# Optimization experiments

Measured on AMD Instinct MI355X. Metric: run time of the kernel, lower is better.

## Reference

```python
import jax, jax.numpy as jnp
import numpy as np

NUM_BITS = 2
QN = -(2 ** (NUM_BITS - 1))          # -2 (signed)
QP = 2 ** (NUM_BITS - 1) - 1         # 1
NUM_LEVELS = 2 ** NUM_BITS           # 4


def setup_inputs() -> dict:
    key = jax.random.key(0)
    k1, k2 = jax.random.split(key)
    # Large transformer FFN weight matrix: d_model=4096, d_ff=16384
    weights = jax.random.normal(k1, (4096, 16384), dtype=jnp.float32) * 0.1
    alpha = jax.random.uniform(k2, (1,), dtype=jnp.float32, minval=0.05, maxval=0.2)
    return {"weights": weights, "alpha": alpha}


def reference(weights, alpha):
    # backprop_to_alpha=False -> alpha is detached everywhere (torch uses .item())
    a = jax.lax.stop_gradient(alpha[0])
    w = weights.reshape(-1)

    # LSQ quantization levels: [Qn*a, ..., -a, 0, a, ..., Qp*a]
    levels = jnp.arange(QN, QP + 1, dtype=w.dtype) * a            # [NUM_LEVELS]

    # Bin assignment by LSQ integer code (non-differentiable indices)
    bins = jnp.round(jnp.clip(w / a, QN, QP)).astype(jnp.int32)   # in [QN, QP]
    idx = bins - QN                                               # in [0, NUM_LEVELS)

    # Single-pass per-bin sum / sumsq / count (replaces per-bin mask loop)
    count = jax.ops.segment_sum(jnp.ones_like(w), idx, num_segments=NUM_LEVELS)
    s = jax.ops.segment_sum(w, idx, num_segments=NUM_LEVELS)
    sq = jax.ops.segment_sum(w * w, idx, num_segments=NUM_LEVELS)

    safe = jnp.maximum(count, 1.0)
    mean = s / safe
    var = sq / safe - mean * mean                                 # biased (unbiased=False)

    total_mse = jnp.sum(jnp.where(count > 0, (mean - levels) ** 2, 0.0))
    total_var = jnp.sum(jnp.where(count >= 2, var, 0.0))
    loss = total_mse + total_var

    # Diagnostics (computed under no_grad in torch)
    wq = bins.astype(w.dtype) * a                                 # quantized weights
    d = jax.lax.stop_gradient(w - wq)
    mean_distance = jnp.mean(jnp.abs(d))
    quantization_mse = jnp.mean(d * d)

    return jnp.stack([loss, total_mse, total_var, quantization_mse, mean_distance])
```

## Files before the change

### kernel.cpp

```cpp
#include <hip/hip_runtime.h>
#include <cstdint>

#define TS 16384
#define NSLOT 16
#define NCH 7
#define NPART 1024
#define PBT 256
#define FLQ 1024


__device__ __forceinline__ int kbin_th(float x, double T1, double T2) {
    double xd = (double)x;
    if (xd >   T1) return 1;
    if (xd >= -T1) return 0;
    if (xd >  -T2) return -1;
    return -2;
}

__device__ __forceinline__ double wred64(double v) {
#pragma unroll
    for (int d = 32; d >= 1; d >>= 1) v += __shfl_xor(v, d, 64);
    return v;
}
__device__ __forceinline__ int wred32i(int v) {
#pragma unroll
    for (int d = 32; d >= 1; d >>= 1) v += __shfl_xor(v, d, 64);
    return v;
}

__device__ __forceinline__ int expo_bits(double A) {
    const long long b = __double_as_longlong(A);
    return (int)((b >> 52) & 0x7FF) - 1023;
}
__device__ __forceinline__ int emin_of(double A0) {
    if (!(A0 > 0.0)) return 12345;
    const int e = expo_bits(A0);
    if (e < -100 || e > 100) return 12345;
    return e;
}

__global__ __launch_bounds__(64) void zero2(double* __restrict__ diag,
        float* __restrict__ chains, double* __restrict__ A0d) {
    if (threadIdx.x < 8) {
        diag[threadIdx.x] = 0.0;
        chains[threadIdx.x] = 0.0f;
        A0d[threadIdx.x] = 0.0;
    }
}

__global__ __launch_bounds__(PBT) void part1(const float* __restrict__ w,
        const float* __restrict__ alpha, int* __restrict__ hist,
        double* __restrict__ diag, long long n, long long nseg)
{
    const float a = alpha[0];
    const double T1 = (double)a * (0.5 + 0x1p-25);
    const double T2 = (double)a * (1.5 - 0x1p-24);
    const long long seg = (long long)blockIdx.x * nseg;
    long long send = seg + nseg; if (send > n) send = n;
    int h0=0,h1=0,h2=0,h3=0;
    double ad=0.0, dd=0.0, s0=0.0;

    for (long long i = seg + (long long)threadIdx.x*4; i < send; i += PBT*4) {
        float4 v;
        if (i + 3 < send) v = *reinterpret_cast<const float4*>(w + i);
        else {
            v = make_float4(0.f,0.f,0.f,0.f);
            v.x = w[i];
            if (i+1 < send) v.y = w[i+1];
            if (i+2 < send) v.z = w[i+2];
        }
        const float xs[4] = {v.x, v.y, v.z, v.w};
        const int nv = (int)((send - i) < 4 ? (send - i) : 4);
#pragma unroll
        for (int j = 0; j < 4; ++j) {
            if (j >= nv) break;
            const float x = xs[j];
            const int k = kbin_th(x, T1, T2);
            h0 += (k==-2); h1 += (k==-1); h2 += (k==0); h3 += (k==1);
            const float bf = (float)k;
            const float wq = __fmul_rn(bf, a);
            const float d  = __fsub_rn(x, wq);
            ad += (double)fabsf(d);
            dd += (double)__fmul_rn(d, d);
            if (k == 0) s0 += (double)x;
        }
    }

    h0 = wred32i(h0); h1 = wred32i(h1); h2 = wred32i(h2); h3 = wred32i(h3);
    ad = wred64(ad);  dd = wred64(dd);  s0 = wred64(s0);

    __shared__ int    ih[4][4];
    __shared__ double dh[4][3];
    const int lane = threadIdx.x & 63, wv = threadIdx.x >> 6;
    if (lane == 0) {
        ih[wv][0]=h0; ih[wv][1]=h1; ih[wv][2]=h2; ih[wv][3]=h3;
        dh[wv][0]=ad; dh[wv][1]=dd; dh[wv][2]=s0;
    }
    __syncthreads();
    if (threadIdx.x < 4)
        hist[blockIdx.x*4 + threadIdx.x] =
            ih[0][threadIdx.x]+ih[1][threadIdx.x]+ih[2][threadIdx.x]+ih[3][threadIdx.x];
    if (threadIdx.x == 4) atomicAdd(&diag[0], dh[0][0]+dh[1][0]+dh[2][0]+dh[3][0]);
    if (threadIdx.x == 5) atomicAdd(&diag[1], dh[0][1]+dh[1][1]+dh[2][1]+dh[3][1]);
    if (threadIdx.x == 6) atomicAdd(&diag[2], dh[0][2]+dh[1][2]+dh[2][2]+dh[3][2]);
}

__global__ __launch_bounds__(256) void scank(const int* __restrict__ hist,
        int* __restrict__ bbase, int* __restrict__ hdr)
{
    const int wv = threadIdx.x >> 6, lane = threadIdx.x & 63;
    if (wv < 4) {
        int running = 0;
        for (int c = 0; c < NPART/64; ++c) {
            int v = hist[(c*64 + lane)*4 + wv];
            int p = v;
#pragma unroll
            for (int d = 1; d < 64; d <<= 1) {
                int t = __shfl_up(p, d, 64);
                if (lane >= d) p += t;
            }
            bbase[(c*64+lane)*4 + wv] = running + p - v;
            running += __shfl(p, 63, 64);
        }
        if (lane == 0) hdr[wv] = running;
    }
    __syncthreads();
    if (threadIdx.x == 0) {
        int b = 0;
        for (int q = 0; q < 4; ++q) { hdr[4+q] = b; b += (hdr[q] + 63) & ~63; }
    }
}

__global__ __launch_bounds__(PBT) void part2(const float* __restrict__ w,
        const float* __restrict__ alpha, const int* __restrict__ bbase,
        const int* __restrict__ hdr, float* __restrict__ streams,
        long long n, long long nseg)
{
    const float a = alpha[0];
    const double T1 = (double)a * (0.5 + 0x1p-25);
    const double T2 = (double)a * (1.5 - 0x1p-24);
    __shared__ float buf[4][2048];
    __shared__ int run[4], fill[4];
    __shared__ int wtot[4][4];
    const int tid = threadIdx.x, wv = tid >> 6, lane = tid & 63;
    if (tid < 4) { run[tid] = hdr[4+tid] + bbase[blockIdx.x*4 + tid]; fill[tid] = 0; }
    __syncthreads();

    const long long seg = (long long)blockIdx.x * nseg;
    long long send = seg + nseg; if (send > n) send = n;

    for (long long base = seg; base < send; base += PBT*4) {
        const long long i = base + (long long)tid * 4;
        float xs[4]; int kk[4];
        int c0=0,c1=0,c2=0,c3=0;
        if (i < send) {
            float4 v;
            if (i + 3 < send) v = *reinterpret_cast<const float4*>(w + i);
            else {
                v = make_float4(0.f,0.f,0.f,0.f);
                v.x = w[i];
                if (i+1 < send) v.y = w[i+1];
                if (i+2 < send) v.z = w[i+2];
            }
            xs[0]=v.x; xs[1]=v.y; xs[2]=v.z; xs[3]=v.w;
            const int nv = (int)((send - i) < 4 ? (send - i) : 4);
#pragma unroll
            for (int j = 0; j < 4; ++j) {
                kk[j] = (j < nv) ? kbin_th(xs[j], T1, T2) : 9;
                c0 += (kk[j]==-2); c1 += (kk[j]==-1);
                c2 += (kk[j]==0);  c3 += (kk[j]==1);
            }
        } else { kk[0]=kk[1]=kk[2]=kk[3]=9; xs[0]=xs[1]=xs[2]=xs[3]=0.f; }

        int p0=c0,p1=c1,p2=c2,p3=c3;
#pragma unroll
        for (int d = 1; d < 64; d <<= 1) {
            int t0=__shfl_up(p0,d,64), t1=__shfl_up(p1,d,64);
            int t2=__shfl_up(p2,d,64), t3=__shfl_up(p3,d,64);
            if (lane >= d) { p0+=t0; p1+=t1; p2+=t2; p3+=t3; }
        }
        const int q0=__shfl(p0,63,64), q1=__shfl(p1,63,64);
        const int q2=__shfl(p2,63,64), q3=__shfl(p3,63,64);
        p0-=c0; p1-=c1; p2-=c2; p3-=c3;
        if (lane == 0) { wtot[wv][0]=q0; wtot[wv][1]=q1; wtot[wv][2]=q2; wtot[wv][3]=q3; }
        __syncthreads();
        int o0=fill[0], o1=fill[1], o2=fill[2], o3=fill[3];
        for (int ww = 0; ww < wv; ++ww) {
            o0+=wtot[ww][0]; o1+=wtot[ww][1]; o2+=wtot[ww][2]; o3+=wtot[ww][3];
        }
        o0+=p0; o1+=p1; o2+=p2; o3+=p3;
#pragma unroll
        for (int j = 0; j < 4; ++j) {
            const int k = kk[j];
            if (k == 9) continue;
            if      (k==-2) buf[0][o0++] = xs[j];
            else if (k==-1) buf[1][o1++] = xs[j];
            else if (k== 0) buf[2][o2++] = xs[j];
            else            buf[3][o3++] = xs[j];
        }
        __syncthreads();
        if (tid < 4) fill[tid] += wtot[0][tid]+wtot[1][tid]+wtot[2][tid]+wtot[3][tid];
        __syncthreads();

#pragma unroll
        for (int b = 0; b < 4; ++b) {
            if (fill[b] >= FLQ) {
                const int rem = fill[b] - FLQ;
#pragma unroll
                for (int r = 0; r < FLQ/PBT; ++r)
                    streams[(long long)run[b] + r*PBT + tid] = buf[b][r*PBT + tid];
                float mv = 0.f;
                if (tid < rem) mv = buf[b][FLQ + tid];
                __syncthreads();
                if (tid < rem) buf[b][tid] = mv;
                if (tid == 0) { run[b] += FLQ; fill[b] = rem; }
                __syncthreads();
            }
        }
    }
#pragma unroll
    for (int b = 0; b < 4; ++b) {
        for (int i2 = tid; i2 < fill[b]; i2 += PBT)
            streams[(long long)run[b] + i2] = buf[b][i2];
    }
}

__device__ void span_st(const float* __restrict__ p, int isq,
                        double& A, long long lo, long long hi, int lane)
{
    for (long long base = lo; base < hi; base += 4096) {
        float xs[64];
        const long long e0 = base + (long long)lane * 64;
#pragma unroll
        for (int q4 = 0; q4 < 16; ++q4) {
            const long long fi = e0 + q4 * 4;
            float4 v = make_float4(0.f,0.f,0.f,0.f);
            if (fi + 3 < hi) v = *reinterpret_cast<const float4*>(p + fi);
            else {
                if (fi     < hi) v.x = p[fi];
                if (fi + 1 < hi) v.y = p[fi + 1];
                if (fi + 2 < hi) v.z = p[fi + 2];
            }
            xs[q4*4+0]=v.x; xs[q4*4+1]=v.y; xs[q4*4+2]=v.z; xs[q4*4+3]=v.w;
        }
#pragma unroll
        for (int j = 0; j < 64; ++j) {
            const float x = xs[j];
            xs[j] = isq ? __fmul_rn(x, x) : fabsf(x);
        }

        int C = 0;
        while (C < 64) {
            if (A > 0.0) {
                const int e = ilogb(A);
                const double u  = ldexp(1.0, e - 23);
                const double Bb = ldexp(1.0, e + 1);
                const double sc = ldexp(1.0, 23 - e);
                double kd = 0.0;
                if (lane >= C) {
#pragma unroll
                    for (int j = 0; j < 64; ++j) kd += rint((double)xs[j] * sc);
                }
                const bool big = kd >= 1099511627776.0;
                double pp = kd;
#pragma unroll
                for (int d = 1; d < 64; d <<= 1) {
                    double tt = __shfl_up(pp, d, 64);
                    if (lane >= d) pp += tt;
                }
                const bool cross = (lane >= C) && (big || (A + u * pp >= Bb));
                const unsigned long long bal = __ballot(cross);
                if (bal == 0ULL) {
                    A = A + u * __shfl(pp, 63);
                    break;
                }
                const int F = __ffsll((long long)bal) - 1;
                double An = 0.0;
                if (lane == F) {
                    const double Aex = A + u * (pp - kd);
                    float Af = (float)Aex;
#pragma unroll
                    for (int j = 0; j < 64; ++j) Af = __fadd_rn(Af, xs[j]);
                    An = (double)Af;
                }
                A = __shfl(An, F);
                C = F + 1;
            } else {
                bool has = false;
                if (lane >= C) {
#pragma unroll
                    for (int j = 0; j < 64; ++j) has = has || (xs[j] > 0.0f);
                }
                const unsigned long long bal = __ballot(has);
                if (bal == 0ULL) break;
                const int F = __ffsll((long long)bal) - 1;
                double An = 0.0;
                if (lane == F) {
                    float Af = 0.0f;
#pragma unroll
                    for (int j = 0; j < 64; ++j) Af = __fadd_rn(Af, xs[j]);
                    An = (double)Af;
                }
                A = __shfl(An, F);
                C = F + 1;
            }
        }
    }
}

__global__ __launch_bounds__(64) void span0(const float* __restrict__ streams,
        const int* __restrict__ hdr, double* __restrict__ A0d)
{
    const int ch = blockIdx.x;
    const int STR[NCH] = {0,1,3,0,1,2,3};
    const int ISQ[NCH] = {0,0,0,1,1,1,1};
    const int st = STR[ch];
    const long long cnt = (long long)hdr[st];
    const float* p = streams + hdr[4+st];
    double A = 0.0;
    if (cnt > 0)
        span_st(p, ISQ[ch], A, 0LL, (TS < cnt ? (long long)TS : cnt), threadIdx.x);
    if (threadIdx.x == 0) A0d[ch] = A;
}

template<int ISQT>
__device__ __forceinline__ void passA_one(const float* __restrict__ p,
        long long cnt, double* __restrict__ krow, long long ntg, long long tile,
        float base)
{
    const long long lo = tile * TS;
    long long hi = lo + TS; if (hi > cnt) hi = cnt;

    float scale[NSLOT];
    scale[0] = base;
#pragma unroll
    for (int s = 1; s < NSLOT; ++s) scale[s] = scale[s-1] * 0.5f;
    int acc[NSLOT];
#pragma unroll
    for (int s = 0; s < NSLOT; ++s) acc[s] = 0;

    const int tid = threadIdx.x;
    for (long long i = lo + (long long)tid*4; i < hi; i += 256*4) {
        float4 v;
        if (i + 3 < hi) v = *reinterpret_cast<const float4*>(p + i);
        else {
            v = make_float4(0.f,0.f,0.f,0.f);
            v.x = p[i];
            if (i+1 < hi) v.y = p[i+1];
            if (i+2 < hi) v.z = p[i+2];
        }
        const float xsv[4] = {v.x, v.y, v.z, v.w};
#pragma unroll
        for (int j = 0; j < 4; ++j) {
            const float x = xsv[j];
            const float xv = ISQT ? __fmul_rn(x, x) : fabsf(x);
#pragma unroll
            for (int s = 0; s < NSLOT; ++s)
                acc[s] += (int)rintf(xv * scale[s]);
        }
    }

    __shared__ double lred[4][NSLOT];
    const int lane = tid & 63, wv = tid >> 6;
#pragma unroll
    for (int s = 0; s < NSLOT; ++s) {
        double r = wred64((double)acc[s]);
        if (lane == 0) lred[wv][s] = r;
    }
    __syncthreads();
    if (tid < NSLOT)
        krow[(long long)tid * ntg + tile] =
            lred[0][tid]+lred[1][tid]+lred[2][tid]+lred[3][tid];
}

__global__ __launch_bounds__(256) void passA7(const float* __restrict__ streams,
        const int* __restrict__ hdr, const double* __restrict__ A0d,
        double* __restrict__ Ktab, long long ntg)
{
    const int ch = blockIdx.y;
    const int STR[NCH] = {0,1,3,0,1,2,3};
    const int st = STR[ch];
    const long long cnt = (long long)hdr[st];
    const long long tile = blockIdx.x;
    if (tile * TS >= cnt) return;
    const int em = emin_of(A0d[ch]);
    const float base = (em == 12345) ? 0.0f : ldexpf(1.0f, 23 - em);
    const float* p = streams + hdr[4+st];
    double* krow = Ktab + (long long)ch * NSLOT * ntg;
    if (ch < 3) passA_one<0>(p, cnt, krow, ntg, tile, base);
    else        passA_one<1>(p, cnt, krow, ntg, tile, base);
}

__global__ __launch_bounds__(64) void walk2(const float* __restrict__ streams,
        const int* __restrict__ hdr, const double* __restrict__ A0d,
        const double* __restrict__ Ktab, float* __restrict__ chains, long long ntg)
{
    const int ch = blockIdx.x;
    const int lane = threadIdx.x;
    const int STR[NCH]  = {0,1,3,0,1,2,3};
    const int ISQ[NCH]  = {0,0,0,1,1,1,1};
    const int OSLOT[NCH]= {0,1,3,4,5,6,7};
    const int st = STR[ch], isq = ISQ[ch];
    const long long cnt = (long long)hdr[st];
    const float* p = streams + hdr[4+st];
    const long long ntiles = (cnt + TS - 1) / TS;
    const double* krow = Ktab + (long long)ch * NSLOT * ntg;
    const int em = emin_of(A0d[ch]);

    double A = A0d[ch];
    long long t = 1;
    while (t < ntiles) {
        if (A > 0.0 && em != 12345) {
            const int e = expo_bits(A);
            const int slot = e - em;
            if (slot >= 0 && slot < NSLOT) {
                const long long wt = t + lane;
                double Kv = (wt < ntiles) ? krow[(long long)slot * ntg + wt] : 0.0;
                double P = Kv;
#pragma unroll
                for (int d = 1; d < 64; d <<= 1) {
                    double tt = __shfl_up(P, d, 64);
                    if (lane >= d) P += tt;
                }
                const double u  = ldexp(1.0, e - 23);
                const double Bb = ldexp(1.0, e + 1);
                const bool bad = (A + u * P > Bb);
                const unsigned long long bal = __ballot(bad);
                if (bal == 0ULL) { A += u * __shfl(P, 63); t += 64; continue; }
                const int F = __ffsll((long long)bal) - 1;
                if (F > 0) { A += u * __shfl(P, F - 1); t += F; }
                const long long lo = t * (long long)TS;
                long long hi = lo + TS; if (hi > cnt) hi = cnt;
                span_st(p, isq, A, lo, hi, lane);
                ++t;
                continue;
            }
        }
        const long long lo = t * (long long)TS;
        long long hi = lo + TS; if (hi > cnt) hi = cnt;
        span_st(p, isq, A, lo, hi, lane);
        ++t;
    }
    if (lane == 0) chains[OSLOT[ch]] = (float)A;
}

__global__ void fin2(const float* __restrict__ chains,
                     const double* __restrict__ diag,
                     const int* __restrict__ hdr,
                     const float* __restrict__ alpha,
                     float* __restrict__ out, long long n)
{
    const float a = alpha[0];
    const float s_np[4]  = { -chains[0], -chains[1], (float)diag[2], chains[3] };
    const float sq_np[4] = {  chains[4],  chains[5],  chains[6],     chains[7] };
    float tmse = 0.f, tvar = 0.f;
#pragma unroll
    for (int b = 0; b < 4; ++b) {
        float cnt = fminf((float)hdr[b], 16777216.0f);
        float safe = fmaxf(cnt, 1.0f);
        float mean = __fdiv_rn(s_np[b], safe);
        float var  = __fsub_rn(__fdiv_rn(sq_np[b], safe), __fmul_rn(mean, mean));
        float lvl  = __fmul_rn((float)(b - 2), a);
        float e    = __fsub_rn(mean, lvl);
        if (cnt > 0.f)  tmse = __fadd_rn(tmse, __fmul_rn(e, e));
        if (cnt >= 2.f) tvar = __fadd_rn(tvar, var);
    }
    out[0] = __fadd_rn(tmse, tvar);
    out[1] = tmse;
    out[2] = tvar;
    out[3] = (float)(diag[1] / (double)n);
    out[4] = (float)(diag[0] / (double)n);
}

__global__ __launch_bounds__(64) void zero_diag6(double* __restrict__ diag) {
    if (threadIdx.x < 6) diag[threadIdx.x] = 0.0;
}
__global__ __launch_bounds__(256) void diag6(const float* __restrict__ w,
        const float* __restrict__ alpha, double* __restrict__ diag, int n4, long long n)
{
    const float a = alpha[0];
    float ad = 0.f, dd = 0.f; int c0=0,c1=0,c2=0,c3=0;
    auto pe = [&](float x) {
        float r = __fdiv_rn(x, a);
        float cl = fminf(1.0f, fmaxf(-2.0f, r));
        float bf = rintf(cl); int k = (int)bf;
        float wq = __fmul_rn(bf, a); float d = __fsub_rn(x, wq);
        ad = __fadd_rn(ad, fabsf(d)); dd = __fadd_rn(dd, __fmul_rn(d, d));
        if (k==-2) c0++; else if (k==-1) c1++; else if (k==0) c2++; else c3++;
    };
    const float4* w4 = reinterpret_cast<const float4*>(w);
    const int stride = gridDim.x * 256;
    for (int i = blockIdx.x * 256 + threadIdx.x; i < n4; i += stride) {
        float4 v = w4[i]; pe(v.x); pe(v.y); pe(v.z); pe(v.w);
    }
    if (blockIdx.x == 0 && threadIdx.x == 0)
        for (long long i = (long long)n4 * 4; i < n; ++i) pe(w[i]);
    double vals[6] = {(double)ad,(double)dd,(double)c0,(double)c1,(double)c2,(double)c3};
    __shared__ double red[256];
    const int tid = threadIdx.x;
#pragma unroll
    for (int j = 0; j < 6; ++j) {
        red[tid] = vals[j]; __syncthreads();
        for (int s = 128; s > 0; s >>= 1) { if (tid < s) red[tid] += red[tid+s]; __syncthreads(); }
        if (tid == 0) atomicAdd(&diag[j], red[0]);
        __syncthreads();
    }
}
__global__ __launch_bounds__(64) void seq_chains(const float* __restrict__ w,
        const float* __restrict__ alpha, float* __restrict__ chains, long long n)
{
    const float a = alpha[0];
    const int lane = threadIdx.x; const int myrow = lane & 7;
    __shared__ float val[8][64];
    float acc = 0.0f;
    const long long ntl = (n + 63) / 64;
    float x_next = (lane < n) ? w[lane] : 0.0f;
    for (long long t = 0; t < ntl; ++t) {
        float x = x_next;
        { long long idxn = (t + 1) * 64 + lane; x_next = (idxn < n) ? w[idxn] : 0.0f; }
        const long long idx = t * 64 + lane;
        const bool valid = (idx < n);
        float r = __fdiv_rn(x, a);
        float cl = fminf(1.0f, fmaxf(-2.0f, r));
        int k = (int)rintf(cl); int row = k + 2;
        float xx = __fmul_rn(x, x);
#pragma unroll
        for (int b = 0; b < 4; ++b) {
            val[b][lane]     = (valid && row == b) ? x  : 0.0f;
            val[4 + b][lane] = (valid && row == b) ? xx : 0.0f;
        }
        __syncthreads();
        if (lane < 8) {
#pragma unroll
            for (int e4i = 0; e4i < 16; ++e4i) {
                float4 v = *reinterpret_cast<const float4*>(&val[myrow][e4i * 4]);
                acc = __fadd_rn(acc, v.x); acc = __fadd_rn(acc, v.y);
                acc = __fadd_rn(acc, v.z); acc = __fadd_rn(acc, v.w);
            }
        }
        __syncthreads();
    }
    if (lane < 8) chains[lane] = acc;
}
__global__ void fin_seq(const float* __restrict__ chains, const double* __restrict__ diag,
                        const float* __restrict__ alpha, float* __restrict__ out, long long n)
{
    const float a = alpha[0];
    float tmse = 0.0f, tvar = 0.0f;
#pragma unroll
    for (int b = 0; b < 4; ++b) {
        float cnt = fminf((float)diag[2 + b], 16777216.0f);
        float safe = fmaxf(cnt, 1.0f);
        float mean = __fdiv_rn(chains[b], safe);
        float var  = __fsub_rn(__fdiv_rn(chains[4 + b], safe), __fmul_rn(mean, mean));
        float lvl  = __fmul_rn((float)(b - 2), a);
        float e    = __fsub_rn(mean, lvl);
        if (cnt > 0.0f)  tmse = __fadd_rn(tmse, __fmul_rn(e, e));
        if (cnt >= 2.0f) tvar = __fadd_rn(tvar, var);
    }
    out[0] = __fadd_rn(tmse, tvar);
    out[1] = tmse; out[2] = tvar;
    out[3] = (float)(diag[1] / (double)n);
    out[4] = (float)(diag[0] / (double)n);
}

extern "C" void kernel_launch(void* const* d_in, const int* in_sizes, int n_in,
                              void* d_out, int out_size, void* d_ws, size_t ws_size,
                              hipStream_t stream) {
    const float* w     = (const float*)d_in[0];
    const float* alpha = (const float*)d_in[1];
    float* out = (float*)d_out;
    const long long n = (long long)in_sizes[0];
    const long long ntg = (n + TS - 1) / TS;

    size_t off = 0;
    const size_t ktab_off = off;   off += (size_t)NCH * NSLOT * ntg * 8;
    const size_t hist_off = off;   off += (size_t)NPART * 4 * 4;
    const size_t bbase_off = off;  off += (size_t)NPART * 4 * 4;
    const size_t hdr_off = off;    off += 8 * 4;
    const size_t diag_off = (off + 7) & ~(size_t)7;  off = diag_off + 8 * 8;
    const size_t a0_off = off;     off += 8 * 8;
    const size_t chains_off = off; off += 8 * 4;
    const size_t streams_off = (off + 255) & ~(size_t)255;
    const size_t need1 = streams_off + ((size_t)n + 512) * 4;

    if (ws_size >= need1) {
        double* Ktab   = (double*)((char*)d_ws + ktab_off);
        int*    hist   = (int*)   ((char*)d_ws + hist_off);
        int*    bbase  = (int*)   ((char*)d_ws + bbase_off);
        int*    hdr    = (int*)   ((char*)d_ws + hdr_off);
        double* diag   = (double*)((char*)d_ws + diag_off);
        double* A0d    = (double*)((char*)d_ws + a0_off);
        float*  chains = (float*) ((char*)d_ws + chains_off);
        float*  strm   = (float*) ((char*)d_ws + streams_off);
        long long nseg = ((n + NPART - 1) / NPART + 1023) & ~1023LL;

        zero2<<<1, 64, 0, stream>>>(diag, chains, A0d);
        part1<<<NPART, PBT, 0, stream>>>(w, alpha, hist, diag, n, nseg);
        scank<<<1, 256, 0, stream>>>(hist, bbase, hdr);
        part2<<<NPART, PBT, 0, stream>>>(w, alpha, bbase, hdr, strm, n, nseg);
        span0<<<NCH, 64, 0, stream>>>(strm, hdr, A0d);
        dim3 ga((unsigned)ntg, NCH);
        passA7<<<ga, 256, 0, stream>>>(strm, hdr, A0d, Ktab, ntg);
        walk2<<<NCH, 64, 0, stream>>>(strm, hdr, A0d, Ktab, chains, ntg);
        fin2<<<1, 1, 0, stream>>>(chains, diag, hdr, alpha, out, n);
    } else {
        float*  chains = (float*)d_ws;
        double* diag   = (double*)((char*)d_ws + 128);
        zero_diag6<<<1, 64, 0, stream>>>(diag);
        diag6<<<1024, 256, 0, stream>>>(w, alpha, diag, (int)(n >> 2), n);
        seq_chains<<<1, 64, 0, stream>>>(w, alpha, chains, n);
        fin_seq<<<1, 1, 0, stream>>>(chains, diag, alpha, out, n);
    }
}
```

Before: 645.8 us.

## Use single-wave partition blocks and fuse sum/sumsq passes per stream

The partition kernels now use 4096 single-wavefront blocks instead of 1024 four-wave blocks. This removes the cross-wave shared-memory scan and several block barriers per iteration, and the flush threshold and buffer size shrink to match. passA now runs one block per stream instead of per channel, so each element is loaded once to accumulate both the |x| and x² slot counters. The slot count drops from 16 to 13, which trades extra per-thread register pressure for fewer global reads, and may change accuracy if walk2 relies on the slot count.

```diff
diff --git a/kernel.cpp b/kernel.cpp
--- a/kernel.cpp
+++ b/kernel.cpp
@@ -2,11 +2,11 @@
 #include <cstdint>
 
 #define TS 16384
-#define NSLOT 16
+#define NSLOT 13
 #define NCH 7
-#define NPART 1024
-#define PBT 256
-#define FLQ 1024
+#define NW 4096
+#define FCAP 1024
+#define FLQ 512
 
 
 __device__ __forceinline__ int kbin_th(float x, double T1, double T2) {
@@ -48,19 +48,20 @@
     }
 }
 
-__global__ __launch_bounds__(PBT) void part1(const float* __restrict__ w,
+__global__ __launch_bounds__(64) void part1(const float* __restrict__ w,
         const float* __restrict__ alpha, int* __restrict__ hist,
-        double* __restrict__ diag, long long n, long long nseg)
+        double* __restrict__ diag, long long n, long long nsegw)
 {
     const float a = alpha[0];
     const double T1 = (double)a * (0.5 + 0x1p-25);
     const double T2 = (double)a * (1.5 - 0x1p-24);
-    const long long seg = (long long)blockIdx.x * nseg;
-    long long send = seg + nseg; if (send > n) send = n;
+    const long long seg = (long long)blockIdx.x * nsegw;
+    long long send = seg + nsegw; if (send > n) send = n;
+    const int lane = threadIdx.x;
     int h0=0,h1=0,h2=0,h3=0;
     double ad=0.0, dd=0.0, s0=0.0;
 
-    for (long long i = seg + (long long)threadIdx.x*4; i < send; i += PBT*4) {
+    for (long long i = seg + (long long)lane*4; i < send; i += 256) {
         float4 v;
         if (i + 3 < send) v = *reinterpret_cast<const float4*>(w + i);
         else {
@@ -89,20 +90,15 @@
     h0 = wred32i(h0); h1 = wred32i(h1); h2 = wred32i(h2); h3 = wred32i(h3);
     ad = wred64(ad);  dd = wred64(dd);  s0 = wred64(s0);
 
-    __shared__ int    ih[4][4];
-    __shared__ double dh[4][3];
-    const int lane = threadIdx.x & 63, wv = threadIdx.x >> 6;
     if (lane == 0) {
-        ih[wv][0]=h0; ih[wv][1]=h1; ih[wv][2]=h2; ih[wv][3]=h3;
-        dh[wv][0]=ad; dh[wv][1]=dd; dh[wv][2]=s0;
-    }
-    __syncthreads();
-    if (threadIdx.x < 4)
-        hist[blockIdx.x*4 + threadIdx.x] =
-            ih[0][threadIdx.x]+ih[1][threadIdx.x]+ih[2][threadIdx.x]+ih[3][threadIdx.x];
-    if (threadIdx.x == 4) atomicAdd(&diag[0], dh[0][0]+dh[1][0]+dh[2][0]+dh[3][0]);
-    if (threadIdx.x == 5) atomicAdd(&diag[1], dh[0][1]+dh[1][1]+dh[2][1]+dh[3][1]);
-    if (threadIdx.x == 6) atomicAdd(&diag[2], dh[0][2]+dh[1][2]+dh[2][2]+dh[3][2]);
+        hist[blockIdx.x*4 + 0] = h0;
+        hist[blockIdx.x*4 + 1] = h1;
+        hist[blockIdx.x*4 + 2] = h2;
+        hist[blockIdx.x*4 + 3] = h3;
+        atomicAdd(&diag[0], ad);
+        atomicAdd(&diag[1], dd);
+        atomicAdd(&diag[2], s0);
+    }
 }
 
 __global__ __launch_bounds__(256) void scank(const int* __restrict__ hist,
@@ -111,7 +107,7 @@
     const int wv = threadIdx.x >> 6, lane = threadIdx.x & 63;
     if (wv < 4) {
         int running = 0;
-        for (int c = 0; c < NPART/64; ++c) {
+        for (int c = 0; c < NW/64; ++c) {
             int v = hist[(c*64 + lane)*4 + wv];
             int p = v;
 #pragma unroll
@@ -131,28 +127,31 @@
     }
 }
 
-__global__ __launch_bounds__(PBT) void part2(const float* __restrict__ w,
+__global__ __launch_bounds__(64) void part2(const float* __restrict__ w,
         const float* __restrict__ alpha, const int* __restrict__ bbase,
         const int* __restrict__ hdr, float* __restrict__ streams,
-        long long n, long long nseg)
+        long long n, long long nsegw)
 {
     const float a = alpha[0];
     const double T1 = (double)a * (0.5 + 0x1p-25);
     const double T2 = (double)a * (1.5 - 0x1p-24);
-    __shared__ float buf[4][2048];
-    __shared__ int run[4], fill[4];
-    __shared__ int wtot[4][4];
-    const int tid = threadIdx.x, wv = tid >> 6, lane = tid & 63;
-    if (tid < 4) { run[tid] = hdr[4+tid] + bbase[blockIdx.x*4 + tid]; fill[tid] = 0; }
-    __syncthreads();
-
-    const long long seg = (long long)blockIdx.x * nseg;
-    long long send = seg + nseg; if (send > n) send = n;
-
-    for (long long base = seg; base < send; base += PBT*4) {
-        const long long i = base + (long long)tid * 4;
+    __shared__ float buf[4][FCAP + 8];
+    const int lane = threadIdx.x;
+
+    int run[4], fill[4];
+#pragma unroll
+    for (int b = 0; b < 4; ++b) {
+        run[b]  = hdr[4+b] + bbase[blockIdx.x*4 + b];
+        fill[b] = 0;
+    }
+
+    const long long seg = (long long)blockIdx.x * nsegw;
+    long long send = seg + nsegw; if (send > n) send = n;
+
+    for (long long base = seg; base < send; base += 256) {
+        const long long i = base + (long long)lane * 4;
         float xs[4]; int kk[4];
-        int c0=0,c1=0,c2=0,c3=0;
+        int c[4] = {0,0,0,0};
         if (i < send) {
             float4 v;
             if (i + 3 < send) v = *reinterpret_cast<const float4*>(w + i);
@@ -167,60 +166,60 @@
 #pragma unroll
             for (int j = 0; j < 4; ++j) {
                 kk[j] = (j < nv) ? kbin_th(xs[j], T1, T2) : 9;
-                c0 += (kk[j]==-2); c1 += (kk[j]==-1);
-                c2 += (kk[j]==0);  c3 += (kk[j]==1);
+                c[0] += (kk[j]==-2); c[1] += (kk[j]==-1);
+                c[2] += (kk[j]==0);  c[3] += (kk[j]==1);
             }
         } else { kk[0]=kk[1]=kk[2]=kk[3]=9; xs[0]=xs[1]=xs[2]=xs[3]=0.f; }
 
-        int p0=c0,p1=c1,p2=c2,p3=c3;
+        int p0=c[0],p1=c[1],p2=c[2],p3=c[3];
 #pragma unroll
         for (int d = 1; d < 64; d <<= 1) {
             int t0=__shfl_up(p0,d,64), t1=__shfl_up(p1,d,64);
             int t2=__shfl_up(p2,d,64), t3=__shfl_up(p3,d,64);
             if (lane >= d) { p0+=t0; p1+=t1; p2+=t2; p3+=t3; }
         }
-        const int q0=__shfl(p0,63,64), q1=__shfl(p1,63,64);
-        const int q2=__shfl(p2,63,64), q3=__shfl(p3,63,64);
-        p0-=c0; p1-=c1; p2-=c2; p3-=c3;
-        if (lane == 0) { wtot[wv][0]=q0; wtot[wv][1]=q1; wtot[wv][2]=q2; wtot[wv][3]=q3; }
-        __syncthreads();
-        int o0=fill[0], o1=fill[1], o2=fill[2], o3=fill[3];
-        for (int ww = 0; ww < wv; ++ww) {
-            o0+=wtot[ww][0]; o1+=wtot[ww][1]; o2+=wtot[ww][2]; o3+=wtot[ww][3];
-        }
-        o0+=p0; o1+=p1; o2+=p2; o3+=p3;
+        const int tot0=__shfl(p0,63,64), tot1=__shfl(p1,63,64);
+        const int tot2=__shfl(p2,63,64), tot3=__shfl(p3,63,64);
+        int o[4] = { fill[0]+p0-c[0], fill[1]+p1-c[1],
+                     fill[2]+p2-c[2], fill[3]+p3-c[3] };
 #pragma unroll
         for (int j = 0; j < 4; ++j) {
             const int k = kk[j];
             if (k == 9) continue;
-            if      (k==-2) buf[0][o0++] = xs[j];
-            else if (k==-1) buf[1][o1++] = xs[j];
-            else if (k== 0) buf[2][o2++] = xs[j];
-            else            buf[3][o3++] = xs[j];
-        }
-        __syncthreads();
-        if (tid < 4) fill[tid] += wtot[0][tid]+wtot[1][tid]+wtot[2][tid]+wtot[3][tid];
+            const int b = k + 2;
+            buf[b][o[b]++] = xs[j];
+        }
+        fill[0]+=tot0; fill[1]+=tot1; fill[2]+=tot2; fill[3]+=tot3;
         __syncthreads();
 
 #pragma unroll
         for (int b = 0; b < 4; ++b) {
             if (fill[b] >= FLQ) {
+#pragma unroll
+                for (int r = 0; r < FLQ/64; ++r)
+                    streams[(long long)run[b] + r*64 + lane] = buf[b][r*64 + lane];
                 const int rem = fill[b] - FLQ;
-#pragma unroll
-                for (int r = 0; r < FLQ/PBT; ++r)
-                    streams[(long long)run[b] + r*PBT + tid] = buf[b][r*PBT + tid];
-                float mv = 0.f;
-                if (tid < rem) mv = buf[b][FLQ + tid];
+                float tmp[4];
+#pragma unroll
+                for (int r = 0; r < 4; ++r) {
+                    const int idx = lane + r*64;
+                    tmp[r] = (idx < rem) ? buf[b][FLQ + idx] : 0.f;
+                }
                 __syncthreads();
-                if (tid < rem) buf[b][tid] = mv;
-                if (tid == 0) { run[b] += FLQ; fill[b] = rem; }
+#pragma unroll
+                for (int r = 0; r < 4; ++r) {
+                    const int idx = lane + r*64;
+                    if (idx < rem) buf[b][idx] = tmp[r];
+                }
+                run[b] += FLQ; fill[b] = rem;
                 __syncthreads();
             }
         }
     }
+    __syncthreads();
 #pragma unroll
     for (int b = 0; b < 4; ++b) {
-        for (int i2 = tid; i2 < fill[b]; i2 += PBT)
+        for (int i2 = lane; i2 < fill[b]; i2 += 64)
             streams[(long long)run[b] + i2] = buf[b][i2];
     }
 }
@@ -323,21 +322,21 @@
     if (threadIdx.x == 0) A0d[ch] = A;
 }
 
-template<int ISQT>
-__device__ __forceinline__ void passA_one(const float* __restrict__ p,
-        long long cnt, double* __restrict__ krow, long long ntg, long long tile,
-        float base)
+template<int HASS>
+__device__ __forceinline__ void passA_two(const float* __restrict__ p,
+        long long cnt, double* __restrict__ krowS, double* __restrict__ krowQ,
+        float baseS, float baseQ, long long ntg, long long tile)
 {
     const long long lo = tile * TS;
     long long hi = lo + TS; if (hi > cnt) hi = cnt;
 
-    float scale[NSLOT];
-    scale[0] = base;
-#pragma unroll
-    for (int s = 1; s < NSLOT; ++s) scale[s] = scale[s-1] * 0.5f;
-    int acc[NSLOT];
-#pragma unroll
-    for (int s = 0; s < NSLOT; ++s) acc[s] = 0;
+    float scS[NSLOT], scQ[NSLOT];
+    scS[0] = baseS; scQ[0] = baseQ;
+#pragma unroll
+    for (int s = 1; s < NSLOT; ++s) { scS[s] = scS[s-1]*0.5f; scQ[s] = scQ[s-1]*0.5f; }
+    int accS[NSLOT], accQ[NSLOT];
+#pragma unroll
+    for (int s = 0; s < NSLOT; ++s) { accS[s] = 0; accQ[s] = 0; }
 
     const int tid = threadIdx.x;
     for (long long i = lo + (long long)tid*4; i < hi; i += 256*4) {
@@ -352,43 +351,65 @@
         const float xsv[4] = {v.x, v.y, v.z, v.w};
 #pragma unroll
         for (int j = 0; j < 4; ++j) {
-            const float x = xsv[j];
-            const float xv = ISQT ? __fmul_rn(x, x) : fabsf(x);
+            const float x  = xsv[j];
+            const float xq = __fmul_rn(x, x);
+            if (HASS) {
+                const float ax = fabsf(x);
+#pragma unroll
+                for (int s = 0; s < NSLOT; ++s)
+                    accS[s] += (int)rintf(ax * scS[s]);
+            }
 #pragma unroll
             for (int s = 0; s < NSLOT; ++s)
-                acc[s] += (int)rintf(xv * scale[s]);
-        }
-    }
-
-    __shared__ double lred[4][NSLOT];
+                accQ[s] += (int)rintf(xq * scQ[s]);
+        }
+    }
+
+    __shared__ double lred[4][2*NSLOT];
     const int lane = tid & 63, wv = tid >> 6;
 #pragma unroll
     for (int s = 0; s < NSLOT; ++s) {
-        double r = wred64((double)acc[s]);
-        if (lane == 0) lred[wv][s] = r;
+        double rs = wred64((double)accS[s]);
+        double rq = wred64((double)accQ[s]);
+        if (lane == 0) { lred[wv][s] = rs; lred[wv][NSLOT+s] = rq; }
     }
     __syncthreads();
-    if (tid < NSLOT)
-        krow[(long long)tid * ntg + tile] =
-            lred[0][tid]+lred[1][tid]+lred[2][tid]+lred[3][tid];
+    if (tid < 2*NSLOT) {
+        const double sum = lred[0][tid]+lred[1][tid]+lred[2][tid]+lred[3][tid];
+        if (tid < NSLOT) {
+            if (HASS) krowS[(long long)tid * ntg + tile] = sum;
+        } else {
+            krowQ[(long long)(tid-NSLOT) * ntg + tile] = sum;
+        }
+    }
 }
 
 __global__ __launch_bounds__(256) void passA7(const float* __restrict__ streams,
         const int* __restrict__ hdr, const double* __restrict__ A0d,
         double* __restrict__ Ktab, long long ntg)
 {
-    const int ch = blockIdx.y;
-    const int STR[NCH] = {0,1,3,0,1,2,3};
-    const int st = STR[ch];
+    const int st = blockIdx.y;
+    const int SCH[4] = {0, 1, -1, 2};
+    const int QCH[4] = {3, 4,  5, 6};
     const long long cnt = (long long)hdr[st];
     const long long tile = blockIdx.x;
     if (tile * TS >= cnt) return;
-    const int em = emin_of(A0d[ch]);
-    const float base = (em == 12345) ? 0.0f : ldexpf(1.0f, 23 - em);
     const float* p = streams + hdr[4+st];
-    double* krow = Ktab + (long long)ch * NSLOT * ntg;
-    if (ch < 3) passA_one<0>(p, cnt, krow, ntg, tile, base);
-    else        passA_one<1>(p, cnt, krow, ntg, tile, base);
+
+    const int qch = QCH[st];
+    const int emQ = emin_of(A0d[qch]);
+    const float baseQ = (emQ == 12345) ? 0.0f : ldexpf(1.0f, 23 - emQ);
+    double* krowQ = Ktab + (long long)qch * NSLOT * ntg;
+
+    if (SCH[st] >= 0) {
+        const int sch = SCH[st];
+        const int emS = emin_of(A0d[sch]);
+        const float baseS = (emS == 12345) ? 0.0f : ldexpf(1.0f, 23 - emS);
+        double* krowS = Ktab + (long long)sch * NSLOT * ntg;
+        passA_two<1>(p, cnt, krowS, krowQ, baseS, baseQ, ntg, tile);
+    } else {
+        passA_two<0>(p, cnt, nullptr, krowQ, 0.0f, baseQ, ntg, tile);
+    }
 }
 
 __global__ __launch_bounds__(64) void walk2(const float* __restrict__ streams,
@@ -575,8 +596,8 @@
 
     size_t off = 0;
     const size_t ktab_off = off;   off += (size_t)NCH * NSLOT * ntg * 8;
-    const size_t hist_off = off;   off += (size_t)NPART * 4 * 4;
-    const size_t bbase_off = off;  off += (size_t)NPART * 4 * 4;
+    const size_t hist_off = off;   off += (size_t)NW * 4 * 4;
+    const size_t bbase_off = off;  off += (size_t)NW * 4 * 4;
     const size_t hdr_off = off;    off += 8 * 4;
     const size_t diag_off = (off + 7) & ~(size_t)7;  off = diag_off + 8 * 8;
     const size_t a0_off = off;     off += 8 * 8;
@@ -593,14 +614,14 @@
         double* A0d    = (double*)((char*)d_ws + a0_off);
         float*  chains = (float*) ((char*)d_ws + chains_off);
         float*  strm   = (float*) ((char*)d_ws + streams_off);
-        long long nseg = ((n + NPART - 1) / NPART + 1023) & ~1023LL;
+        long long nsegw = ((n + NW - 1) / NW + 7) & ~7LL;
 
         zero2<<<1, 64, 0, stream>>>(diag, chains, A0d);
-        part1<<<NPART, PBT, 0, stream>>>(w, alpha, hist, diag, n, nseg);
+        part1<<<NW, 64, 0, stream>>>(w, alpha, hist, diag, n, nsegw);
         scank<<<1, 256, 0, stream>>>(hist, bbase, hdr);
-        part2<<<NPART, PBT, 0, stream>>>(w, alpha, bbase, hdr, strm, n, nseg);
+        part2<<<NW, 64, 0, stream>>>(w, alpha, bbase, hdr, strm, n, nsegw);
         span0<<<NCH, 64, 0, stream>>>(strm, hdr, A0d);
-        dim3 ga((unsigned)ntg, NCH);
+        dim3 ga((unsigned)ntg, 4);
         passA7<<<ga, 256, 0, stream>>>(strm, hdr, A0d, Ktab, ntg);
         walk2<<<NCH, 64, 0, stream>>>(strm, hdr, A0d, Ktab, chains, ntg);
         fin2<<<1, 1, 0, stream>>>(chains, diag, hdr, alpha, out, n);
```

After: 768.3 us. +19.0%, slower.
